# Kernel optimization log

Hardware: AMD Instinct MI355X
Metric: run time of the kernel (lower is better)

Reference implementation:

```python
import jax, jax.numpy as jnp
import numpy as np

D = 2048      # d_model
H = 32        # n_heads
DS = 64       # d_state = d_model // n_heads
K = 4         # conv kernel size (hardcoded in module)
EPS = 1e-6


def setup_inputs() -> dict:
    key = jax.random.key(0)
    ks = jax.random.split(key, 8)
    B, L = 2, 4096
    s = lambda k, shp, sc: jax.random.normal(k, shp, dtype=jnp.float32) * sc
    return {
        "x": s(ks[0], (B, L, D), 1.0),
        "state": jnp.zeros((B, H, DS), jnp.float32),
        "norm_w": jnp.ones((D,), jnp.float32),
        "conv_w": s(ks[1], (D, K), 0.5),          # depthwise conv weight [d_model, K]
        "conv_b": s(ks[2], (D,), 0.1),
        "pp_w": s(ks[3], (D, 3 * H * DS), 0.02),  # param_proj (stored [in, out])
        "pp_b": jnp.zeros((3 * H * DS,), jnp.float32),
        "gp_w": s(ks[4], (D, D), 0.02),           # gate_proj
        "gp_b": jnp.zeros((D,), jnp.float32),
        "op_w": s(ks[5], (D, D), 0.02),           # out_proj
        "op_b": jnp.zeros((D,), jnp.float32),
    }


def reference(x, state, norm_w, conv_w, conv_b, pp_w, pp_b, gp_w, gp_b, op_w, op_b):
    B, L, Dm = x.shape
    # RMSNorm
    rms = jnp.sqrt(jnp.mean(x * x, axis=-1, keepdims=True) + EPS)
    xn = norm_w * x / rms
    # causal depthwise conv1d + SiLU (pad left K-1, valid cross-correlation)
    xp = jnp.pad(xn, ((0, 0), (K - 1, 0), (0, 0)))
    xc = conv_b + sum(xp[:, k:k + L, :] * conv_w[:, k] for k in range(K))
    xc = jax.nn.silu(xc)
    gate = jax.nn.sigmoid(xc @ gp_w + gp_b)                  # [B, L, D]
    p = (xn @ pp_w + pp_b).reshape(B, L, H, 3, DS)
    delta = jax.nn.sigmoid(p[..., 0, :])                     # [B, L, H, DS]
    Bm, Cm = p[..., 1, :], p[..., 2, :]
    # sequential recurrence h_t = delta_t * h_{t-1} + B_t, time-major scan
    dt = jnp.moveaxis(delta, 1, 0)                           # [L, B, H, DS]
    Bt = jnp.moveaxis(Bm, 1, 0)
    def step(h, db):
        d, b = db
        h = d * h + b
        return h, h
    h_last, hs = jax.lax.scan(step, state, (dt, Bt))         # hs: [L, B, H, DS]
    ssm = (jnp.moveaxis(Cm, 1, 0) * hs).reshape(L, B, Dm)
    ssm = jnp.moveaxis(ssm, 0, 1)                            # [B, L, D]
    mixed = gate * ssm + (1.0 - gate) * xn
    y = mixed @ op_w + op_b + x
    return y, h_last
```

## Files before the change

kernel.cpp:

```cpp
#include <hip/hip_runtime.h>
#include <math.h>

#define BB   2
#define LL   4096
#define DD   2048
#define HH   32
#define DSS  64
#define MM   (BB * LL)
#define N3   (3 * HH * DSS)
#define NCH  64
#define CLN  64
#define EPSF 1e-6f
#define TR_NBX 320
#define TR_NBY (DD / 32)
#define NT   (DD / 64)
#define GT_NB (DD / 256)
#define PJ_NB (N3 / 256)

typedef unsigned short bf16;
typedef __attribute__((ext_vector_type(8))) short bf16x8;
typedef __attribute__((ext_vector_type(4))) float f32x4;

__device__ __forceinline__ float bf2f(bf16 u) {
    union { unsigned int i; float f; } v;
    v.i = ((unsigned int)u) << 16;
    return v.f;
}
__device__ __forceinline__ bf16 f2bf(float f) {
    union { float f; unsigned int u; } v;
    v.f = f;
    unsigned int r = (v.u >> 16) & 1u;
    return (bf16)((v.u + 0x7fffu + r) >> 16);
}
__device__ __forceinline__ float sigmoidf_(float v) {
    return 1.0f / (1.0f + __expf(-v));
}
__device__ __forceinline__ void gload16(const void* g, void* l) {
    __builtin_amdgcn_global_load_lds(
        (const __attribute__((address_space(1))) void*)g,
        (__attribute__((address_space(3))) void*)l, 16, 0, 0);
}

#define SBAR()  asm volatile("s_barrier" ::: "memory")
#define VMC(n)  asm volatile("s_waitcnt vmcnt(" #n ")" ::: "memory")

__global__ __launch_bounds__(256) void rms_transpose(const float* __restrict__ x,
                                                     const float* __restrict__ w,
                                                     bf16* __restrict__ xn,
                                                     const float* __restrict__ gp_w,
                                                     const float* __restrict__ op_w,
                                                     const float* __restrict__ pp_w,
                                                     bf16* __restrict__ gp_wT,
                                                     bf16* __restrict__ op_wT,
                                                     bf16* __restrict__ pp_wT) {
    __shared__ float sh[32 * 33];
    int t = threadIdx.x;
    if (blockIdx.x < MM) {
        int row = blockIdx.x;
        const float4* x4 = (const float4*)(x + (size_t)row * DD);
        ushort4* o4 = (ushort4*)(xn + (size_t)row * DD);
        const float4* w4 = (const float4*)w;
        float4 v0 = x4[t], v1 = x4[t + 256];
        float ss = v0.x * v0.x + v0.y * v0.y + v0.z * v0.z + v0.w * v0.w +
                   v1.x * v1.x + v1.y * v1.y + v1.z * v1.z + v1.w * v1.w;
#pragma unroll
        for (int off = 32; off >= 1; off >>= 1) ss += __shfl_down(ss, off, 64);
        if ((t & 63) == 0) sh[t >> 6] = ss;
        __syncthreads();
        float tot = sh[0] + sh[1] + sh[2] + sh[3];
        float inv = 1.0f / sqrtf(tot * (1.0f / DD) + EPSF);
        float4 wa = w4[t], wb = w4[t + 256];
        ushort4 r0, r1;
        r0.x = f2bf(v0.x * inv * wa.x); r0.y = f2bf(v0.y * inv * wa.y);
        r0.z = f2bf(v0.z * inv * wa.z); r0.w = f2bf(v0.w * inv * wa.w);
        r1.x = f2bf(v1.x * inv * wb.x); r1.y = f2bf(v1.y * inv * wb.y);
        r1.z = f2bf(v1.z * inv * wb.z); r1.w = f2bf(v1.w * inv * wb.w);
        o4[t] = r0; o4[t + 256] = r1;
    } else {
        int id = blockIdx.x - MM;
        int bx = id % TR_NBX;
        int k0 = (id / TR_NBX) << 5;
        const float* W; bf16* WT; int Ndim;
        if (bx < 64)       { W = gp_w; WT = gp_wT; Ndim = DD; }
        else if (bx < 128) { W = op_w; WT = op_wT; Ndim = DD; bx -= 64; }
        else               { W = pp_w; WT = pp_wT; Ndim = N3; bx -= 128; }
        int n0 = bx << 5;
        float (*tl)[33] = (float (*)[33])sh;
        int tx = t & 31, ty = t >> 5;
#pragma unroll
        for (int i = 0; i < 32; i += 8)
            tl[ty + i][tx] = W[(size_t)(k0 + ty + i) * Ndim + n0 + tx];
        __syncthreads();
        int tx2 = t & 15, ty2 = t >> 4;
#pragma unroll
        for (int i = 0; i < 32; i += 16) {
            int n = ty2 + i;
            ushort2 v = { f2bf(tl[tx2 * 2][n]), f2bf(tl[tx2 * 2 + 1][n]) };
            *(ushort2*)&WT[(size_t)(n0 + n) * DD + k0 + tx2 * 2] = v;
        }
    }
}

#define CONV_LC 16
__global__ __launch_bounds__(256) void conv_silu_kernel(const bf16* __restrict__ xn,
                                                        const float* __restrict__ cw,
                                                        const float* __restrict__ cb,
                                                        bf16* __restrict__ xc) {
    int b = blockIdx.z;
    int l0 = blockIdx.x * CONV_LC;
    int d0 = blockIdx.y * 1024 + threadIdx.x * 4;
    float4 w[4];
    float bias[4];
#pragma unroll
    for (int j = 0; j < 4; ++j) {
        w[j] = ((const float4*)cw)[d0 + j];
        bias[j] = cb[d0 + j];
    }
    float win[3][4];
#pragma unroll
    for (int k = 0; k < 3; ++k) {
        int l = l0 - 3 + k;
        if (l >= 0) {
            ushort4 v = *(const ushort4*)&xn[((size_t)b * LL + l) * DD + d0];
            win[k][0] = bf2f(v.x); win[k][1] = bf2f(v.y);
            win[k][2] = bf2f(v.z); win[k][3] = bf2f(v.w);
        } else {
            win[k][0] = win[k][1] = win[k][2] = win[k][3] = 0.0f;
        }
    }
    size_t off = ((size_t)b * LL + l0) * DD + d0;
#pragma unroll 4
    for (int i = 0; i < CONV_LC; ++i) {
        ushort4 v = *(const ushort4*)&xn[off];
        float cur[4] = {bf2f(v.x), bf2f(v.y), bf2f(v.z), bf2f(v.w)};
        ushort4 o;
#pragma unroll
        for (int j = 0; j < 4; ++j) {
            float acc = bias[j] + win[0][j] * w[j].x + win[1][j] * w[j].y +
                        win[2][j] * w[j].z + cur[j] * w[j].w;
            float s = acc * sigmoidf_(acc);
            ((unsigned short*)&o)[j] = f2bf(s);
        }
        *(ushort4*)&xc[off] = o;
#pragma unroll
        for (int j = 0; j < 4; ++j) {
            win[0][j] = win[1][j]; win[1][j] = win[2][j]; win[2][j] = cur[j];
        }
        off += DD;
    }
}

template <int EPI, typename OutT>
__device__ __forceinline__ void gemm_tile256(const bf16* __restrict__ A,
                                             const bf16* __restrict__ Bt,
                                             const float* __restrict__ bias,
                                             const float* __restrict__ add,
                                             OutT* __restrict__ out,
                                             int Ndim, int m0, int n0,
                                             bf16* lds) {
    const int tid  = threadIdx.x;
    const int wave = tid >> 6;
    const int lane = tid & 63;
    const int sr   = lane >> 3;
    const int gcol = ((lane & 7) ^ sr) << 3;
    const bf16* gA = A  + (size_t)(m0 + wave * 16 + sr) * DD + gcol;
    const bf16* gB = Bt + (size_t)(n0 + wave * 16 + sr) * DD + gcol;
    const int ldst = wave * 1024 + lane * 8;

    const int fr = lane & 15;
    const int kg = lane >> 4;
    const int f7 = fr & 7;
    const int wm = (wave >> 2) << 6;
    const int wn = (wave & 3) << 5;

    auto STAGE = [&](int bufsel, int half, int tau) {
        const bf16* src = (half < 2 ? gA : gB) +
                          (size_t)((half & 1) << 7) * DD + tau * 64;
        bf16* dst = lds + bufsel * 32768 + half * 8192 + ldst;
        gload16(src, dst);
        gload16(src + 8 * DD, dst + 512);
    };

    f32x4 acc[8][4] = {};
    bf16x8 af[4][2], b0[2][2], b1[2][2];

    STAGE(0, 0, 0); STAGE(0, 3, 0); STAGE(0, 1, 0); STAGE(0, 2, 0);
    STAGE(1, 0, 1); STAGE(1, 3, 1);
    VMC(4);
    SBAR();

#pragma unroll 2
    for (int tau = 0; tau < NT; ++tau) {
        const int bsel = tau & 1;
        bf16* Ls = lds + bsel * 32768;
#pragma unroll
        for (int i = 0; i < 4; ++i)
#pragma unroll
            for (int ks = 0; ks < 2; ++ks)
                af[i][ks] = *(const bf16x8*)&Ls[(wm + i * 16 + fr) * 64 +
                                               ((((ks << 2) | kg) ^ f7) << 3)];
#pragma unroll
        for (int j = 0; j < 2; ++j)
#pragma unroll
            for (int ks = 0; ks < 2; ++ks)
                b0[j][ks] = *(const bf16x8*)&Ls[2 * 8192 + (wn + j * 16 + fr) * 64 +
                                               ((((ks << 2) | kg) ^ f7) << 3)];
#pragma unroll
        for (int j = 0; j < 2; ++j)
#pragma unroll
            for (int ks = 0; ks < 2; ++ks)
                b1[j][ks] = *(const bf16x8*)&Ls[3 * 8192 + (wn + j * 16 + fr) * 64 +
                                               ((((ks << 2) | kg) ^ f7) << 3)];
        if (tau + 1 < NT) { STAGE(bsel ^ 1, 1, tau + 1); STAGE(bsel ^ 1, 2, tau + 1); }
        SBAR();
        __builtin_amdgcn_sched_barrier(0);
        __builtin_amdgcn_s_setprio(1);
#pragma unroll
        for (int ks = 0; ks < 2; ++ks)
#pragma unroll
            for (int i = 0; i < 4; ++i)
#pragma unroll
                for (int j = 0; j < 2; ++j)
                    acc[i][j] = __builtin_amdgcn_mfma_f32_16x16x32_bf16(
                        af[i][ks], b0[j][ks], acc[i][j], 0, 0, 0);
        __builtin_amdgcn_s_setprio(0);
        __builtin_amdgcn_sched_barrier(0);
        SBAR();
        if (tau + 2 < NT) STAGE(bsel, 0, tau + 2);
        SBAR();
        __builtin_amdgcn_sched_barrier(0);
        __builtin_amdgcn_s_setprio(1);
#pragma unroll
        for (int ks = 0; ks < 2; ++ks)
#pragma unroll
            for (int i = 0; i < 4; ++i)
#pragma unroll
                for (int j = 0; j < 2; ++j)
                    acc[i][2 + j] = __builtin_amdgcn_mfma_f32_16x16x32_bf16(
                        af[i][ks], b1[j][ks], acc[i][2 + j], 0, 0, 0);
        __builtin_amdgcn_s_setprio(0);
        __builtin_amdgcn_sched_barrier(0);
#pragma unroll
        for (int i = 0; i < 4; ++i)
#pragma unroll
            for (int ks = 0; ks < 2; ++ks)
                af[i][ks] = *(const bf16x8*)&Ls[8192 + (wm + i * 16 + fr) * 64 +
                                               ((((ks << 2) | kg) ^ f7) << 3)];
        SBAR();
        if (tau + 2 < NT) STAGE(bsel, 3, tau + 2);
        if (tau < NT - 2) { VMC(4); } else { VMC(0); }
        SBAR();
        __builtin_amdgcn_sched_barrier(0);
        __builtin_amdgcn_s_setprio(1);
#pragma unroll
        for (int ks = 0; ks < 2; ++ks)
#pragma unroll
            for (int i = 0; i < 4; ++i)
#pragma unroll
                for (int j = 0; j < 2; ++j)
                    acc[4 + i][2 + j] = __builtin_amdgcn_mfma_f32_16x16x32_bf16(
                        af[i][ks], b1[j][ks], acc[4 + i][2 + j], 0, 0, 0);
#pragma unroll
        for (int ks = 0; ks < 2; ++ks)
#pragma unroll
            for (int i = 0; i < 4; ++i)
#pragma unroll
                for (int j = 0; j < 2; ++j)
                    acc[4 + i][j] = __builtin_amdgcn_mfma_f32_16x16x32_bf16(
                        af[i][ks], b0[j][ks], acc[4 + i][j], 0, 0, 0);
        __builtin_amdgcn_s_setprio(0);
        __builtin_amdgcn_sched_barrier(0);
        SBAR();
    }

    const int baseRow = m0 + wm + (kg << 2);
    const int baseCol = n0 + wn + fr;
    float bia[4];
#pragma unroll
    for (int nf = 0; nf < 4; ++nf)
        bia[nf] = bias[baseCol + (nf >> 1) * 128 + (nf & 1) * 16];
#pragma unroll
    for (int mf = 0; mf < 8; ++mf) {
#pragma unroll
        for (int r = 0; r < 4; ++r) {
            int m = baseRow + (mf >> 2) * 128 + (mf & 3) * 16 + r;
            size_t rowoff = (size_t)m * Ndim + baseCol;
#pragma unroll
            for (int nf = 0; nf < 4; ++nf) {
                size_t off = rowoff + (nf >> 1) * 128 + (nf & 1) * 16;
                float v = acc[mf][nf][r] + bia[nf];
                if (EPI == 1) v = sigmoidf_(v);
                if (EPI == 2) v += add[off];
                if constexpr (sizeof(OutT) == 4)
                    ((float*)out)[off] = v;
                else
                    ((bf16*)out)[off] = f2bf(v);
            }
        }
    }
}

__global__ __launch_bounds__(512, 2) void gemm_gateproj(const bf16* __restrict__ xc,
                                                        const bf16* __restrict__ gp_wT,
                                                        const float* __restrict__ gp_b,
                                                        bf16* __restrict__ gate,
                                                        const bf16* __restrict__ xn,
                                                        const bf16* __restrict__ pp_wT,
                                                        const float* __restrict__ pp_b,
                                                        bf16* __restrict__ p) {
    __shared__ __align__(16) bf16 lds[2 * 4 * 8192];
    int fid = blockIdx.x;
    int f = (fid & 7) * 128 + (fid >> 3);
    int by = f >> 5;
    int bx = f & 31;
    int m0 = by << 8;
    if (bx < GT_NB)
        gemm_tile256<1, bf16>(xc, gp_wT, gp_b, nullptr, gate, DD,
                              m0, bx << 8, lds);
    else
        gemm_tile256<0, bf16>(xn, pp_wT, pp_b, nullptr, p, N3,
                              m0, (bx - GT_NB) << 8, lds);
}

__global__ __launch_bounds__(512, 2) void gemm_out(const bf16* __restrict__ mixed,
                                                   const bf16* __restrict__ op_wT,
                                                   const float* __restrict__ op_b,
                                                   const float* __restrict__ x,
                                                   float* __restrict__ y) {
    __shared__ __align__(16) bf16 lds[2 * 4 * 8192];
    int fid = blockIdx.x;
    int f = (fid & 7) * 32 + (fid >> 3);
    int m0 = (f >> 3) << 8;
    int n0 = (f & 7) << 8;
    gemm_tile256<2, float>(mixed, op_wT, op_b, x, y, DD, m0, n0, lds);
}


__global__ __launch_bounds__(256) void scan_phase1(const bf16* __restrict__ p,
                                                   float* __restrict__ cA,
                                                   float* __restrict__ cB) {
    int c = blockIdx.x, b = blockIdx.z, s = threadIdx.x & 63;
    int h = blockIdx.y * 4 + (threadIdx.x >> 6);
    size_t base = ((size_t)(b * LL + c * CLN)) * N3 + h * (3 * DSS) + s;
    float a = 1.0f, bb = 0.0f;
#pragma unroll 8
    for (int i = 0; i < CLN; ++i) {
        float d = sigmoidf_(bf2f(p[base]));
        float Bv = bf2f(p[base + DSS]);
        a *= d;
        bb = d * bb + Bv;
        base += N3;
    }
    int idx = ((b * HH + h) * NCH + c) * DSS + s;
    cA[idx] = a;
    cB[idx] = bb;
}

__global__ __launch_bounds__(256) void scan_phase3(const bf16* __restrict__ p,
                                                   const float* __restrict__ cA,
                                                   const float* __restrict__ cB,
                                                   const float* __restrict__ state,
                                                   const bf16* __restrict__ gate,
                                                   const bf16* __restrict__ xn,
                                                   bf16* __restrict__ mixed,
                                                   float* __restrict__ hlast) {
    int c = blockIdx.x, b = blockIdx.z, s = threadIdx.x & 63;
    int h = blockIdx.y * 4 + (threadIdx.x >> 6);
    float hp = state[(b * HH + h) * DSS + s];
    int cbase = ((b * HH + h) * NCH) * DSS + s;
    for (int cc = 0; cc < c; ++cc)
        hp = cA[cbase + cc * DSS] * hp + cB[cbase + cc * DSS];
    size_t prow = ((size_t)(b * LL + c * CLN)) * N3 + h * (3 * DSS) + s;
    size_t grow = ((size_t)(b * LL + c * CLN)) * DD + h * DSS + s;
#pragma unroll 4
    for (int i = 0; i < CLN; ++i) {
        float d = sigmoidf_(bf2f(p[prow]));
        float Bv = bf2f(p[prow + DSS]);
        float Cv = bf2f(p[prow + 2 * DSS]);
        hp = d * hp + Bv;
        float ssm = Cv * hp;
        float g = bf2f(gate[grow]);
        float xv = bf2f(xn[grow]);
        mixed[grow] = f2bf(g * ssm + (1.0f - g) * xv);
        prow += N3;
        grow += DD;
    }
    if (c == NCH - 1) hlast[(b * HH + h) * DSS + s] = hp;
}

extern "C" void kernel_launch(void* const* d_in, const int* in_sizes, int n_in,
                              void* d_out, int out_size, void* d_ws, size_t ws_size,
                              hipStream_t stream) {
    const float* x      = (const float*)d_in[0];
    const float* state  = (const float*)d_in[1];
    const float* norm_w = (const float*)d_in[2];
    const float* conv_w = (const float*)d_in[3];
    const float* conv_b = (const float*)d_in[4];
    const float* pp_w   = (const float*)d_in[5];
    const float* pp_b   = (const float*)d_in[6];
    const float* gp_w   = (const float*)d_in[7];
    const float* gp_b   = (const float*)d_in[8];
    const float* op_w   = (const float*)d_in[9];
    const float* op_b   = (const float*)d_in[10];

    float* y     = (float*)d_out;
    float* hlast = y + (size_t)MM * DD;

    const size_t BHND = (size_t)BB * HH * NCH * DSS;
    char* ws = (char*)d_ws;
    bf16* xn    = (bf16*)ws;
    bf16* xcbuf = xn + (size_t)MM * DD;
    bf16* p     = xcbuf + (size_t)MM * DD;
    float* cA   = (float*)(p + (size_t)MM * N3);
    float* cB   = cA + BHND;
    bf16* gp_wT = (bf16*)(cB + BHND);
    bf16* op_wT = gp_wT + (size_t)DD * DD;
    bf16* gate  = (bf16*)y;
    bf16* pp_wT = gate + (size_t)MM * DD;
    bf16* mixed = xcbuf;

    rms_transpose<<<MM + TR_NBX * TR_NBY, 256, 0, stream>>>(
        x, norm_w, xn, gp_w, op_w, pp_w, gp_wT, op_wT, pp_wT);
    conv_silu_kernel<<<dim3(LL / CONV_LC, DD / 1024, BB), 256, 0, stream>>>(
        xn, conv_w, conv_b, xcbuf);
    gemm_gateproj<<<(GT_NB + PJ_NB) * (MM / 256), 512, 0, stream>>>(
        xcbuf, gp_wT, gp_b, gate, xn, pp_wT, pp_b, p);
    scan_phase1<<<dim3(NCH, HH / 4, BB), 256, 0, stream>>>(p, cA, cB);
    scan_phase3<<<dim3(NCH, HH / 4, BB), 256, 0, stream>>>(
        p, cA, cB, state, gate, xn, mixed, hlast);
    gemm_out<<<MM / 256 * (DD / 256), 512, 0, stream>>>(mixed, op_wT, op_b, x, y);
}
```

Measured before the change: 569.7 us.

## Add separate chunk-prefix scan kernel and vectorize scan loads to two lanes

Adds a scan_phase2 kernel that computes each chunk's starting state once and stores it in a buffer that reuses the gp_wT workspace after the gate GEMM. Previously every phase-3 block serially recomputed the carry over all earlier chunks. Phase 1 and phase 3 now handle two state elements per thread with ushort2/float2 loads, which halves the grid and widens memory accesses. The cost is one extra launch, a small serial kernel, and an extra round trip of the per-chunk state buffer through memory.

```diff
diff --git a/kernel.cpp b/kernel.cpp
--- a/kernel.cpp
+++ b/kernel.cpp
@@ -339,53 +339,77 @@
 __global__ __launch_bounds__(256) void scan_phase1(const bf16* __restrict__ p,
                                                    float* __restrict__ cA,
                                                    float* __restrict__ cB) {
-    int c = blockIdx.x, b = blockIdx.z, s = threadIdx.x & 63;
-    int h = blockIdx.y * 4 + (threadIdx.x >> 6);
-    size_t base = ((size_t)(b * LL + c * CLN)) * N3 + h * (3 * DSS) + s;
-    float a = 1.0f, bb = 0.0f;
+    int c = blockIdx.x, b = blockIdx.z;
+    int h = blockIdx.y * 8 + (threadIdx.x >> 5);
+    int sp = (threadIdx.x & 31) * 2;
+    size_t base = ((size_t)(b * LL + c * CLN)) * N3 + h * (3 * DSS) + sp;
+    float a0 = 1.0f, b0 = 0.0f, a1 = 1.0f, b1 = 0.0f;
 #pragma unroll 8
     for (int i = 0; i < CLN; ++i) {
-        float d = sigmoidf_(bf2f(p[base]));
-        float Bv = bf2f(p[base + DSS]);
-        a *= d;
-        bb = d * bb + Bv;
+        ushort2 dv = *(const ushort2*)&p[base];
+        ushort2 Bv = *(const ushort2*)&p[base + DSS];
+        float d0 = sigmoidf_(bf2f(dv.x));
+        float d1 = sigmoidf_(bf2f(dv.y));
+        a0 *= d0; b0 = d0 * b0 + bf2f(Bv.x);
+        a1 *= d1; b1 = d1 * b1 + bf2f(Bv.y);
         base += N3;
     }
-    int idx = ((b * HH + h) * NCH + c) * DSS + s;
-    cA[idx] = a;
-    cB[idx] = bb;
-}
-
-__global__ __launch_bounds__(256) void scan_phase3(const bf16* __restrict__ p,
-                                                   const float* __restrict__ cA,
+    int idx = ((b * HH + h) * NCH + c) * DSS + sp;
+    *(float2*)&cA[idx] = make_float2(a0, a1);
+    *(float2*)&cB[idx] = make_float2(b0, b1);
+}
+
+__global__ __launch_bounds__(256) void scan_phase2(const float* __restrict__ cA,
                                                    const float* __restrict__ cB,
                                                    const float* __restrict__ state,
+                                                   float* __restrict__ hp0) {
+    int b = blockIdx.z;
+    int s = threadIdx.x & 63;
+    int h = blockIdx.y * 4 + (threadIdx.x >> 6);
+    float hp = state[(b * HH + h) * DSS + s];
+    int base = ((b * HH + h) * NCH) * DSS + s;
+#pragma unroll 8
+    for (int cc = 0; cc < NCH; ++cc) {
+        hp0[base + cc * DSS] = hp;
+        hp = cA[base + cc * DSS] * hp + cB[base + cc * DSS];
+    }
+}
+
+__global__ __launch_bounds__(256) void scan_phase3(const bf16* __restrict__ p,
+                                                   const float* __restrict__ hp0,
                                                    const bf16* __restrict__ gate,
                                                    const bf16* __restrict__ xn,
                                                    bf16* __restrict__ mixed,
                                                    float* __restrict__ hlast) {
-    int c = blockIdx.x, b = blockIdx.z, s = threadIdx.x & 63;
-    int h = blockIdx.y * 4 + (threadIdx.x >> 6);
-    float hp = state[(b * HH + h) * DSS + s];
-    int cbase = ((b * HH + h) * NCH) * DSS + s;
-    for (int cc = 0; cc < c; ++cc)
-        hp = cA[cbase + cc * DSS] * hp + cB[cbase + cc * DSS];
-    size_t prow = ((size_t)(b * LL + c * CLN)) * N3 + h * (3 * DSS) + s;
-    size_t grow = ((size_t)(b * LL + c * CLN)) * DD + h * DSS + s;
+    int c = blockIdx.x, b = blockIdx.z;
+    int h = blockIdx.y * 8 + (threadIdx.x >> 5);
+    int sp = (threadIdx.x & 31) * 2;
+    float2 hp = *(const float2*)&hp0[((b * HH + h) * NCH + c) * DSS + sp];
+    size_t prow = ((size_t)(b * LL + c * CLN)) * N3 + h * (3 * DSS) + sp;
+    size_t grow = ((size_t)(b * LL + c * CLN)) * DD + h * DSS + sp;
 #pragma unroll 4
     for (int i = 0; i < CLN; ++i) {
-        float d = sigmoidf_(bf2f(p[prow]));
-        float Bv = bf2f(p[prow + DSS]);
-        float Cv = bf2f(p[prow + 2 * DSS]);
-        hp = d * hp + Bv;
-        float ssm = Cv * hp;
-        float g = bf2f(gate[grow]);
-        float xv = bf2f(xn[grow]);
-        mixed[grow] = f2bf(g * ssm + (1.0f - g) * xv);
+        ushort2 dv = *(const ushort2*)&p[prow];
+        ushort2 Bv = *(const ushort2*)&p[prow + DSS];
+        ushort2 Cv = *(const ushort2*)&p[prow + 2 * DSS];
+        float d0 = sigmoidf_(bf2f(dv.x));
+        float d1 = sigmoidf_(bf2f(dv.y));
+        hp.x = d0 * hp.x + bf2f(Bv.x);
+        hp.y = d1 * hp.y + bf2f(Bv.y);
+        float ssm0 = bf2f(Cv.x) * hp.x;
+        float ssm1 = bf2f(Cv.y) * hp.y;
+        ushort2 gv = *(const ushort2*)&gate[grow];
+        ushort2 xv = *(const ushort2*)&xn[grow];
+        float g0 = bf2f(gv.x), g1 = bf2f(gv.y);
+        ushort2 o;
+        o.x = f2bf(g0 * ssm0 + (1.0f - g0) * bf2f(xv.x));
+        o.y = f2bf(g1 * ssm1 + (1.0f - g1) * bf2f(xv.y));
+        *(ushort2*)&mixed[grow] = o;
         prow += N3;
         grow += DD;
     }
-    if (c == NCH - 1) hlast[(b * HH + h) * DSS + s] = hp;
+    if (c == NCH - 1)
+        *(float2*)&hlast[(b * HH + h) * DSS + sp] = hp;
 }
 
 extern "C" void kernel_launch(void* const* d_in, const int* in_sizes, int n_in,
@@ -418,6 +442,7 @@
     bf16* gate  = (bf16*)y;
     bf16* pp_wT = gate + (size_t)MM * DD;
     bf16* mixed = xcbuf;
+    float* hp0  = (float*)gp_wT;
 
     rms_transpose<<<MM + TR_NBX * TR_NBY, 256, 0, stream>>>(
         x, norm_w, xn, gp_w, op_w, pp_w, gp_wT, op_wT, pp_wT);
@@ -425,8 +450,9 @@
         xn, conv_w, conv_b, xcbuf);
     gemm_gateproj<<<(GT_NB + PJ_NB) * (MM / 256), 512, 0, stream>>>(
         xcbuf, gp_wT, gp_b, gate, xn, pp_wT, pp_b, p);
-    scan_phase1<<<dim3(NCH, HH / 4, BB), 256, 0, stream>>>(p, cA, cB);
-    scan_phase3<<<dim3(NCH, HH / 4, BB), 256, 0, stream>>>(
-        p, cA, cB, state, gate, xn, mixed, hlast);
+    scan_phase1<<<dim3(NCH, HH / 8, BB), 256, 0, stream>>>(p, cA, cB);
+    scan_phase2<<<dim3(1, HH / 4, BB), 256, 0, stream>>>(cA, cB, state, hp0);
+    scan_phase3<<<dim3(NCH, HH / 8, BB), 256, 0, stream>>>(
+        p, hp0, gate, xn, mixed, hlast);
     gemm_out<<<MM / 256 * (DD / 256), 512, 0, stream>>>(mixed, op_wT, op_b, x, y);
 }
```

Measured after the change: 564.4 us. About the same (-0.9%).
